# Performance work log

Hardware: AMD Instinct MI355X
Metric: run time of the kernel (lower is better)

The kernel has to match this reference:

```python
import jax, jax.numpy as jnp
import numpy as np
import itertools

B, T, N, F, H = 8, 16, 64, 16, 128  # batch, window, num_nodes, node_feat_dim, hidden_dim


def setup_inputs() -> dict:
    key = jax.random.key(0)
    ks = jax.random.split(key, 10)
    # fully-dense directed edge list: all permutations (i, j), i != j -> [2, E]
    ei = np.array([p for p in itertools.permutations(range(N), 2)], dtype=np.int32).T

    def rn(k, shape, scale=0.05):
        return jax.random.normal(k, shape, jnp.float32) * scale

    return dict(
        x_seq=rn(ks[0], (B, T, N, F), 1.0),
        edge_index=jnp.asarray(ei),
        Wg=rn(ks[1], (H, F)), bg=jnp.zeros((H,), jnp.float32),            # self.gcn
        W1=rn(ks[2], (H, 2 * H)), b1=jnp.zeros((H,), jnp.float32),        # edge_predictor[0]
        W2=rn(ks[3], (1, H)), b2=jnp.zeros((1,), jnp.float32),            # edge_predictor[2]
        Wgcn=rn(ks[4], (H, H)), bgcn=jnp.zeros((H,), jnp.float32),        # edge_weighted_gcn.linear
        Wih=rn(ks[5], (3 * H, H * N)), Whh=rn(ks[6], (3 * H, H)),         # GRU
        bih=jnp.zeros((3 * H,), jnp.float32), bhh=jnp.zeros((3 * H,), jnp.float32),
        Wp=rn(ks[7], (1, H)), bp=jnp.zeros((1,), jnp.float32),            # pressure_predictor
    )


def reference(x_seq, edge_index, Wg, bg, W1, b1, W2, b2, Wgcn, bgcn,
              Wih, Whh, bih, bhh, Wp, bp):
    Bv, Tv, Nv, Fv = x_seq.shape
    Hv = Wg.shape[0]
    src, tgt = edge_index[0], edge_index[1]

    # per-timestep node embeddings: self.gcn(x_t), vectorized over (B, T)
    node = jnp.einsum('btnf,hf->btnh', x_seq, Wg) + bg            # [B,T,N,H]

    # edge predictor on concat([emb[src], emb[tgt]]): split W1 to avoid the 2H concat
    W1s, W1t = W1[:, :Hv], W1[:, Hv:]
    eh = (jnp.einsum('bteh,kh->btek', node[:, :, src], W1s)
          + jnp.einsum('bteh,kh->btek', node[:, :, tgt], W1t) + b1)  # [B,T,E,H]
    ew = (jax.nn.relu(eh) @ W2.T + b2)[..., 0]                        # [B,T,E]

    # edge-weighted GCN: out[b,t,tgt] += w[b,t,e] * Linear(node[b,t,src])
    lin = jnp.einsum('btnh,kh->btnk', node, Wgcn) + bgcn              # [B,T,N,H]
    msg = ew[..., None] * lin[:, :, src]                              # [B,T,E,H]
    gcn_out = jnp.zeros((Bv, Tv, Nv, Hv), x_seq.dtype).at[:, :, tgt].add(msg)

    # GRU over time (its output is computed by the module but unused in the returns)
    gru_in = gcn_out.reshape(Bv, Tv, Nv * Hv)

    def step(h, x_t):
        gi = x_t @ Wih.T + bih
        gh = h @ Whh.T + bhh
        ir, iz, inn = jnp.split(gi, 3, -1)
        hr, hz, hn = jnp.split(gh, 3, -1)
        r = jax.nn.sigmoid(ir + hr)
        z = jax.nn.sigmoid(iz + hz)
        n = jnp.tanh(inn + r * hn)
        h_new = (1.0 - z) * n + z * h
        return h_new, h_new

    h0 = jnp.zeros((Bv, Hv), x_seq.dtype)
    _, _gru_out = jax.lax.scan(step, h0, jnp.swapaxes(gru_in, 0, 1))

    pressures = (gcn_out[:, -1] @ Wp.T + bp)[..., 0]                  # [B,N]
    return pressures, ew[:, -1]
```

## Files before the change

### kernel.cpp

```cpp
#include <hip/hip_runtime.h>


#define BB 8
#define TT 16
#define NN 64
#define FF 16
#define HH 128
#define EE 4032

__global__ __launch_bounds__(256) void k_node(const float* __restrict__ x,
                                              const float* __restrict__ Wg,
                                              const float* __restrict__ bg,
                                              float* __restrict__ nodeT) {
  __shared__ float xT[FF * NN];
  __shared__ float wg[HH * FF];
  const int b = blockIdx.x, tid = threadIdx.x;
  const float* xb = x + ((size_t)b * TT + (TT - 1)) * NN * FF;
#pragma unroll
  for (int it = 0; it < 4; ++it) {
    int i = it * 256 + tid;
    xT[(i & 15) * NN + (i >> 4)] = xb[i];
  }
#pragma unroll
  for (int it = 0; it < 8; ++it) {
    int i = it * 256 + tid;
    wg[i] = Wg[i];
  }
  __syncthreads();
  float* out = nodeT + (size_t)b * HH * NN;
#pragma unroll
  for (int it = 0; it < 8; ++it) {
    int g = it * 256 + tid;
    int n0 = (g & 15) * 4, h = g >> 4;
    float bias = bg[h];
    float4 acc = {bias, bias, bias, bias};
#pragma unroll
    for (int f = 0; f < FF; ++f) {
      const float4 xv = *(const float4*)&xT[f * NN + n0];
      const float w = wg[h * FF + f];
      acc.x += xv.x * w; acc.y += xv.y * w; acc.z += xv.z * w; acc.w += xv.w * w;
    }
    *(float4*)&out[h * NN + n0] = acc;
  }
}

__global__ __launch_bounds__(256) void k_gemm(const float* __restrict__ nodeT,
                                              const float* __restrict__ W1,
                                              const float* __restrict__ Wgcn,
                                              const float* __restrict__ bgcn,
                                              float* __restrict__ nsT,
                                              float* __restrict__ ntT,
                                              float* __restrict__ lin) {
  __shared__ float wt[16 * HH];
  const int b = blockIdx.x, m = blockIdx.y;
  const int mat = m >> 3, kq = m & 7, k0 = kq * 16;
  const int tid = threadIdx.x;
  const float* Wsrc;
  int ldw, off;
  if (mat == 0)      { Wsrc = W1;   ldw = 2 * HH; off = 0;  }
  else if (mat == 1) { Wsrc = W1;   ldw = 2 * HH; off = HH; }
  else               { Wsrc = Wgcn; ldw = HH;     off = 0;  }
#pragma unroll
  for (int it = 0; it < 8; ++it) {
    int i = it * 256 + tid;
    int kk = i >> 7, h = i & 127;
    wt[i] = Wsrc[(size_t)(k0 + kk) * ldw + off + h];
  }
  __syncthreads();
  const int row = tid & 63, kg = tid >> 6;
  const float* nb = nodeT + (size_t)b * HH * NN;
  float acc[4];
#pragma unroll
  for (int kk = 0; kk < 4; ++kk)
    acc[kk] = (mat == 2) ? bgcn[k0 + kg * 4 + kk] : 0.f;
  for (int h4 = 0; h4 < 32; ++h4) {
    float nv[4];
#pragma unroll
    for (int u = 0; u < 4; ++u) nv[u] = nb[(h4 * 4 + u) * NN + row];
#pragma unroll
    for (int kk = 0; kk < 4; ++kk) {
      const float4 w4 = *(const float4*)&wt[(kg * 4 + kk) * HH + h4 * 4];
      acc[kk] += nv[0] * w4.x + nv[1] * w4.y + nv[2] * w4.z + nv[3] * w4.w;
    }
  }
  if (mat == 2) {
    float4 v = {acc[0], acc[1], acc[2], acc[3]};
    *(float4*)&lin[((size_t)b * NN + row) * HH + k0 + kg * 4] = v;
  } else {
    float* dst = (mat == 0) ? nsT : ntT;
#pragma unroll
    for (int kk = 0; kk < 4; ++kk)
      dst[((size_t)b * HH + k0 + kg * 4 + kk) * NN + row] = acc[kk];
  }
}

__global__ __launch_bounds__(128) void k_fused(const float* __restrict__ nsT,
                                               const float* __restrict__ ntT,
                                               const float* __restrict__ lin,
                                               const float* __restrict__ b1,
                                               const float* __restrict__ W2,
                                               const float* __restrict__ b2,
                                               const float* __restrict__ Wp,
                                               const float* __restrict__ bp,
                                               float* __restrict__ out) {
  __shared__ float cs[HH], ct[HH], b1s[HH], w2s[HH], ewin[NN];
  __shared__ float red[2];
  const int bx = blockIdx.x, b = bx >> 6, n = bx & 63, tid = threadIdx.x;
  const float* nsb = nsT + (size_t)b * HH * NN;
  const float* ntb = ntT + (size_t)b * HH * NN;
  cs[tid]  = nsb[tid * NN + n];
  ct[tid]  = ntb[tid * NN + n];
  b1s[tid] = b1[tid];
  w2s[tid] = W2[tid];
  __syncthreads();
  const float b2v = b2[0];
  const int wv = tid >> 6, j = tid & 63;
  if (j < 63) {
    const int o = j + (j >= n ? 1 : 0);
    const float* oth = (wv == 0) ? ntb : nsb;
    const float* com = (wv == 0) ? cs : ct;
    float acc = 0.f;
#pragma unroll 4
    for (int k = 0; k < HH; ++k) {
      float v = com[k] + oth[k * NN + o] + b1s[k];
      acc += fmaxf(v, 0.f) * w2s[k];
    }
    acc += b2v;
    if (wv == 0) out[512 + (size_t)b * EE + n * 63 + j] = acc;
    else ewin[j] = acc;
  }
  __syncthreads();
  const float* linb = lin + (size_t)b * NN * HH;
  float acc2 = 0.f;
#pragma unroll 4
  for (int jj = 0; jj < 63; ++jj) {
    int s = jj + (jj >= n ? 1 : 0);
    acc2 += ewin[jj] * linb[s * HH + tid];
  }
  float p = acc2 * Wp[tid];
#pragma unroll
  for (int off = 32; off; off >>= 1) p += __shfl_down(p, off, 64);
  if (j == 0) red[wv] = p;
  __syncthreads();
  if (tid == 0) out[(size_t)b * NN + n] = red[0] + red[1] + bp[0];
}

extern "C" void kernel_launch(void* const* d_in, const int* in_sizes, int n_in,
                              void* d_out, int out_size, void* d_ws, size_t ws_size,
                              hipStream_t stream) {
  const float* x    = (const float*)d_in[0];
  const float* Wg   = (const float*)d_in[2];
  const float* bg   = (const float*)d_in[3];
  const float* W1   = (const float*)d_in[4];
  const float* b1   = (const float*)d_in[5];
  const float* W2   = (const float*)d_in[6];
  const float* b2   = (const float*)d_in[7];
  const float* Wgcn = (const float*)d_in[8];
  const float* bgcn = (const float*)d_in[9];
  const float* Wp   = (const float*)d_in[14];
  const float* bp   = (const float*)d_in[15];

  float* ws    = (float*)d_ws;
  float* nodeT = ws;
  float* nsT   = ws + 65536;
  float* ntT   = ws + 131072;
  float* lin   = ws + 196608;

  k_node<<<BB, 256, 0, stream>>>(x, Wg, bg, nodeT);
  k_gemm<<<dim3(BB, 24), 256, 0, stream>>>(nodeT, W1, Wgcn, bgcn, nsT, ntT, lin);
  k_fused<<<BB * NN, 128, 0, stream>>>(nsT, ntT, lin, b1, W2, b2, Wp, bp,
                                       (float*)d_out);
}
```

Before: 112.4 us.

## Fuse node embedding into projection GEMM kernel and batch loads in fused kernel

Merges the node-embedding kernel into the projection GEMM kernel. Each block now recomputes the last-timestep node embeddings in shared memory instead of reading them from a global buffer, which removes one launch and a global round trip at the cost of redundant recomputation across 24 blocks per batch. The fused kernel also folds b1 into the cached source and target rows, and batches its strided global loads into 16-wide register arrays to expose more memory-level parallelism. Weight loads switch to float4.

```diff
diff --git a/kernel.cpp b/kernel.cpp
--- a/kernel.cpp
+++ b/kernel.cpp
@@ -8,67 +8,71 @@
 #define HH 128
 #define EE 4032
 
-__global__ __launch_bounds__(256) void k_node(const float* __restrict__ x,
+__global__ __launch_bounds__(256) void k_prep(const float* __restrict__ x,
                                               const float* __restrict__ Wg,
                                               const float* __restrict__ bg,
-                                              float* __restrict__ nodeT) {
-  __shared__ float xT[FF * NN];
-  __shared__ float wg[HH * FF];
-  const int b = blockIdx.x, tid = threadIdx.x;
-  const float* xb = x + ((size_t)b * TT + (TT - 1)) * NN * FF;
-#pragma unroll
-  for (int it = 0; it < 4; ++it) {
-    int i = it * 256 + tid;
-    xT[(i & 15) * NN + (i >> 4)] = xb[i];
-  }
-#pragma unroll
-  for (int it = 0; it < 8; ++it) {
-    int i = it * 256 + tid;
-    wg[i] = Wg[i];
-  }
-  __syncthreads();
-  float* out = nodeT + (size_t)b * HH * NN;
-#pragma unroll
-  for (int it = 0; it < 8; ++it) {
-    int g = it * 256 + tid;
-    int n0 = (g & 15) * 4, h = g >> 4;
-    float bias = bg[h];
-    float4 acc = {bias, bias, bias, bias};
-#pragma unroll
-    for (int f = 0; f < FF; ++f) {
-      const float4 xv = *(const float4*)&xT[f * NN + n0];
-      const float w = wg[h * FF + f];
-      acc.x += xv.x * w; acc.y += xv.y * w; acc.z += xv.z * w; acc.w += xv.w * w;
-    }
-    *(float4*)&out[h * NN + n0] = acc;
-  }
-}
-
-__global__ __launch_bounds__(256) void k_gemm(const float* __restrict__ nodeT,
                                               const float* __restrict__ W1,
                                               const float* __restrict__ Wgcn,
                                               const float* __restrict__ bgcn,
                                               float* __restrict__ nsT,
                                               float* __restrict__ ntT,
                                               float* __restrict__ lin) {
-  __shared__ float wt[16 * HH];
-  const int b = blockIdx.x, m = blockIdx.y;
-  const int mat = m >> 3, kq = m & 7, k0 = kq * 16;
-  const int tid = threadIdx.x;
+  __shared__ float node[HH * NN];
+  __shared__ float buf[3072];
+  const int b = blockIdx.x, m = blockIdx.y, tid = threadIdx.x;
+  const int mat = m >> 3, k0 = (m & 7) * 16;
+
+  {
+    float* xT = buf;
+    float* wg = buf + 1024;
+    const float* xb = x + ((size_t)b * TT + (TT - 1)) * NN * FF;
+    {
+      const int i4 = tid * 4;
+      const float4 xv = *(const float4*)&xb[i4];
+      const float* xs = (const float*)&xv;
+#pragma unroll
+      for (int j = 0; j < 4; ++j) {
+        int i = i4 + j;
+        xT[(i & 15) * NN + (i >> 4)] = xs[j];
+      }
+      const int i8 = tid * 8;
+      *(float4*)&wg[i8] = *(const float4*)&Wg[i8];
+      *(float4*)&wg[i8 + 4] = *(const float4*)&Wg[i8 + 4];
+    }
+    __syncthreads();
+#pragma unroll
+    for (int it = 0; it < 8; ++it) {
+      int g = it * 256 + tid;
+      int n0 = (g & 15) * 4, h = g >> 4;
+      float bias = bg[h];
+      float4 acc = {bias, bias, bias, bias};
+#pragma unroll
+      for (int f = 0; f < FF; ++f) {
+        const float4 xv = *(const float4*)&xT[f * NN + n0];
+        const float w = wg[h * FF + f];
+        acc.x += xv.x * w; acc.y += xv.y * w; acc.z += xv.z * w; acc.w += xv.w * w;
+      }
+      *(float4*)&node[h * NN + n0] = acc;
+    }
+  }
+  __syncthreads();
+
+  float* wt = buf;
   const float* Wsrc;
   int ldw, off;
   if (mat == 0)      { Wsrc = W1;   ldw = 2 * HH; off = 0;  }
   else if (mat == 1) { Wsrc = W1;   ldw = 2 * HH; off = HH; }
   else               { Wsrc = Wgcn; ldw = HH;     off = 0;  }
-#pragma unroll
-  for (int it = 0; it < 8; ++it) {
-    int i = it * 256 + tid;
-    int kk = i >> 7, h = i & 127;
-    wt[i] = Wsrc[(size_t)(k0 + kk) * ldw + off + h];
-  }
-  __syncthreads();
+  {
+    const int i8 = tid * 8;
+    const int kk = i8 >> 7, h0 = i8 & 127;
+    const float* src = &Wsrc[(size_t)(k0 + kk) * ldw + off + h0];
+    *(float4*)&wt[i8] = *(const float4*)&src[0];
+    *(float4*)&wt[i8 + 4] = *(const float4*)&src[4];
+  }
+  __syncthreads();
+
   const int row = tid & 63, kg = tid >> 6;
-  const float* nb = nodeT + (size_t)b * HH * NN;
   float acc[4];
 #pragma unroll
   for (int kk = 0; kk < 4; ++kk)
@@ -76,7 +80,7 @@
   for (int h4 = 0; h4 < 32; ++h4) {
     float nv[4];
 #pragma unroll
-    for (int u = 0; u < 4; ++u) nv[u] = nb[(h4 * 4 + u) * NN + row];
+    for (int u = 0; u < 4; ++u) nv[u] = node[(h4 * 4 + u) * NN + row];
 #pragma unroll
     for (int kk = 0; kk < 4; ++kk) {
       const float4 w4 = *(const float4*)&wt[(kg * 4 + kk) * HH + h4 * 4];
@@ -103,27 +107,35 @@
                                                const float* __restrict__ Wp,
                                                const float* __restrict__ bp,
                                                float* __restrict__ out) {
-  __shared__ float cs[HH], ct[HH], b1s[HH], w2s[HH], ewin[NN];
+  __shared__ float csb[HH], ctb[HH], w2s[HH], ewin[NN];
   __shared__ float red[2];
   const int bx = blockIdx.x, b = bx >> 6, n = bx & 63, tid = threadIdx.x;
   const float* nsb = nsT + (size_t)b * HH * NN;
   const float* ntb = ntT + (size_t)b * HH * NN;
-  cs[tid]  = nsb[tid * NN + n];
-  ct[tid]  = ntb[tid * NN + n];
-  b1s[tid] = b1[tid];
-  w2s[tid] = W2[tid];
+  {
+    const float bv = b1[tid];
+    csb[tid] = nsb[tid * NN + n] + bv;
+    ctb[tid] = ntb[tid * NN + n] + bv;
+    w2s[tid] = W2[tid];
+  }
   __syncthreads();
   const float b2v = b2[0];
   const int wv = tid >> 6, j = tid & 63;
   if (j < 63) {
     const int o = j + (j >= n ? 1 : 0);
     const float* oth = (wv == 0) ? ntb : nsb;
-    const float* com = (wv == 0) ? cs : ct;
+    const float* com = (wv == 0) ? csb : ctb;
     float acc = 0.f;
-#pragma unroll 4
-    for (int k = 0; k < HH; ++k) {
-      float v = com[k] + oth[k * NN + o] + b1s[k];
-      acc += fmaxf(v, 0.f) * w2s[k];
+#pragma unroll
+    for (int kb = 0; kb < HH; kb += 16) {
+      float ov[16];
+#pragma unroll
+      for (int u = 0; u < 16; ++u) ov[u] = oth[(kb + u) * NN + o];
+#pragma unroll
+      for (int u = 0; u < 16; ++u) {
+        float v = com[kb + u] + ov[u];
+        acc += fmaxf(v, 0.f) * w2s[kb + u];
+      }
     }
     acc += b2v;
     if (wv == 0) out[512 + (size_t)b * EE + n * 63 + j] = acc;
@@ -132,10 +144,26 @@
   __syncthreads();
   const float* linb = lin + (size_t)b * NN * HH;
   float acc2 = 0.f;
-#pragma unroll 4
-  for (int jj = 0; jj < 63; ++jj) {
-    int s = jj + (jj >= n ? 1 : 0);
-    acc2 += ewin[jj] * linb[s * HH + tid];
+#pragma unroll
+  for (int j0 = 0; j0 < 48; j0 += 16) {
+    float lv[16];
+#pragma unroll
+    for (int u = 0; u < 16; ++u) {
+      int jj = j0 + u, s = jj + (jj >= n ? 1 : 0);
+      lv[u] = linb[s * HH + tid];
+    }
+#pragma unroll
+    for (int u = 0; u < 16; ++u) acc2 += ewin[j0 + u] * lv[u];
+  }
+  {
+    float lv[15];
+#pragma unroll
+    for (int u = 0; u < 15; ++u) {
+      int jj = 48 + u, s = jj + (jj >= n ? 1 : 0);
+      lv[u] = linb[s * HH + tid];
+    }
+#pragma unroll
+    for (int u = 0; u < 15; ++u) acc2 += ewin[48 + u] * lv[u];
   }
   float p = acc2 * Wp[tid];
 #pragma unroll
@@ -160,14 +188,13 @@
   const float* Wp   = (const float*)d_in[14];
   const float* bp   = (const float*)d_in[15];
 
-  float* ws    = (float*)d_ws;
-  float* nodeT = ws;
-  float* nsT   = ws + 65536;
-  float* ntT   = ws + 131072;
-  float* lin   = ws + 196608;
-
-  k_node<<<BB, 256, 0, stream>>>(x, Wg, bg, nodeT);
-  k_gemm<<<dim3(BB, 24), 256, 0, stream>>>(nodeT, W1, Wgcn, bgcn, nsT, ntT, lin);
+  float* ws  = (float*)d_ws;
+  float* nsT = ws;
+  float* ntT = ws + 65536;
+  float* lin = ws + 131072;
+
+  k_prep<<<dim3(BB, 24), 256, 0, stream>>>(x, Wg, bg, W1, Wgcn, bgcn,
+                                           nsT, ntT, lin);
   k_fused<<<BB * NN, 128, 0, stream>>>(nsT, ntT, lin, b1, W2, b2, Wp, bp,
                                        (float*)d_out);
 }
```

New measurement: 104.2 us. 1.08x faster.
